# Optimization experiments

Hardware: AMD Instinct MI355X
Metric: run time of the kernel (lower is better)

Reference implementation:

```python
import jax, jax.numpy as jnp
import numpy as np

N, DIM = 65536, 512

def setup_inputs() -> dict:
    key = jax.random.key(0)
    k1, k2, k3 = jax.random.split(key, 3)
    x = jax.random.normal(k1, (N, DIM), dtype=jnp.float32)
    x_fit = jax.random.normal(k2, (N, DIM), dtype=jnp.float32)
    # Module registers S_inv = eye(dim); add a small symmetric PSD perturbation
    # so the matrix is non-trivial while staying well-conditioned.
    A = jax.random.normal(k3, (DIM, DIM), dtype=jnp.float32) / jnp.float32(DIM)
    S_inv = jnp.eye(DIM, dtype=jnp.float32) + A @ A.T
    return {"x": x, "x_fit": x_fit, "S_inv": S_inv}

def reference(x, x_fit, S_inv):
    # Squared Mahalanobis distance per row:
    # diag(delta @ S_inv @ delta.T) == sum((delta @ S_inv) * delta, axis=-1)
    delta = x - x_fit                      # [N, d]
    return jnp.einsum('nd,de,ne->n', delta, S_inv, delta)  # [N]
```

## Files before the change

kernel.cpp:

```cpp
#include <hip/hip_runtime.h>
#include <stdint.h>

#define DIM 512
#define ROWS_PER_BLOCK 64
#define N_CHUNKS 32
#define CHUNK_BYTES 8192
#define WS_BYTES (N_CHUNKS * CHUNK_BYTES)

typedef __attribute__((ext_vector_type(4))) float f32x4;
typedef __attribute__((ext_vector_type(2))) float f32x2;
typedef __attribute__((ext_vector_type(4))) int   i32x4;

static __device__ __forceinline__ int kperm(int kk, int q) {
  int g = q >> 3, j = q & 7;
  int r = (j < 4) ? (g * 4 + j) : (16 + g * 4 + (j - 4));
  return kk * 32 + r;
}

__global__ void prep_R(const float* __restrict__ S, uint32_t* __restrict__ ws) {
  int idx = blockIdx.x * blockDim.x + threadIdx.x;
  if (idx >= WS_BYTES / 4) return;
  int b     = idx * 4;
  int chunk = b >> 13;
  int e_l   = (b >> 9) & 15;
  int inrow = b & 511;
  int slot  = inrow >> 4;
  int bia   = inrow & 15;
  int la    = (slot - e_l) & 31;
  int P = la >> 2, g = la & 3;
  int e = chunk * 16 + e_l;
  float v[4];
#pragma unroll
  for (int t = 0; t < 4; ++t) {
    int bb = bia + t;
    int j  = bb & 7;
    int kk = 2 * P + (bb >> 3);
    int k  = kperm(kk, g * 8 + j);
    v[t] = 64.0f * (S[k * DIM + e] - (k == e ? 1.0f : 0.0f));
  }
  int w = __builtin_amdgcn_cvt_pk_fp8_f32(v[0], v[1], 0, false);
  w     = __builtin_amdgcn_cvt_pk_fp8_f32(v[2], v[3], w, true);
  ws[idx] = (uint32_t)w;
}

static __device__ __forceinline__ void stage_chunk(const uint32_t* __restrict__ ws,
                                                   int eb, char* dst, int tid) {
  const uint32_t* src = ws + (size_t)eb * (CHUNK_BYTES / 4);
#pragma unroll
  for (int r = 0; r < 2; ++r) {
    int idx = r * 256 + tid;
    __builtin_amdgcn_global_load_lds(
        (const __attribute__((address_space(1))) void*)(src + idx * 4),
        (__attribute__((address_space(3))) void*)(dst + idx * 16),
        16, 0, 0);
  }
}

template <int KK>
struct P0 {
  static __device__ __forceinline__ void run(const float* __restrict__ xr,
                                             const float* __restrict__ fr,
                                             int g, long long (&fragL)[16], float& sumsq) {
    const float4 a0 = *(const float4*)(xr + KK * 32 + 4 * g);
    const float4 b0 = *(const float4*)(fr + KK * 32 + 4 * g);
    const float4 a1 = *(const float4*)(xr + KK * 32 + 16 + 4 * g);
    const float4 b1 = *(const float4*)(fr + KK * 32 + 16 + 4 * g);
    float d0 = a0.x - b0.x, d1 = a0.y - b0.y, d2 = a0.z - b0.z, d3 = a0.w - b0.w;
    float d4 = a1.x - b1.x, d5 = a1.y - b1.y, d6 = a1.z - b1.z, d7 = a1.w - b1.w;
    sumsq += d0*d0 + d1*d1 + d2*d2 + d3*d3 + d4*d4 + d5*d5 + d6*d6 + d7*d7;
    int lo = __builtin_amdgcn_cvt_pk_fp8_f32(d0, d1, 0, false);
    lo     = __builtin_amdgcn_cvt_pk_fp8_f32(d2, d3, lo, true);
    int hi = __builtin_amdgcn_cvt_pk_fp8_f32(d4, d5, 0, false);
    hi     = __builtin_amdgcn_cvt_pk_fp8_f32(d6, d7, hi, true);
    fragL[KK] = (long long)(((unsigned long long)(unsigned)hi << 32) | (unsigned)lo);
    P0<KK + 1>::run(xr, fr, g, fragL, sumsq);
  }
};
template <>
struct P0<16> {
  static __device__ __forceinline__ void run(const float*, const float*, int,
                                             long long (&)[16], float&) {}
};

template <int P>
struct KLoop {
  static __device__ __forceinline__ void run(const char* __restrict__ rowbase,
                                             int g, int m,
                                             const long long (&fragL)[16],
                                             f32x4& c0, f32x4& c1) {
    int off = ((4 * P + g + m) & 31) * 16;
    i32x4 a = *(const i32x4*)(rowbase + off);
    long long A0 = (long long)(((unsigned long long)(unsigned)a[1] << 32) | (unsigned)a[0]);
    long long A1 = (long long)(((unsigned long long)(unsigned)a[3] << 32) | (unsigned)a[2]);
    c0 = __builtin_amdgcn_mfma_f32_16x16x32_fp8_fp8(A0, fragL[2 * P],     c0, 0, 0, 0);
    c1 = __builtin_amdgcn_mfma_f32_16x16x32_fp8_fp8(A1, fragL[2 * P + 1], c1, 0, 0, 0);
    KLoop<P + 1>::run(rowbase, g, m, fragL, c0, c1);
  }
};
template <>
struct KLoop<8> {
  static __device__ __forceinline__ void run(const char*, int, int,
                                             const long long (&)[16], f32x4&, f32x4&) {}
};

template <int EB>
struct ChunkLoop {
  static __device__ __forceinline__ void run(const uint32_t* __restrict__ ws,
                                             char* sA0, char* sA1,
                                             int tid, int m, int g,
                                             const long long (&fragL)[16], float& part) {
    char* cur = (EB & 1) ? sA1 : sA0;
    char* nxt = (EB & 1) ? sA0 : sA1;
    if (EB + 1 < N_CHUNKS) stage_chunk(ws, EB + 1, nxt, tid);

    f32x4 c0 = {0.f, 0.f, 0.f, 0.f}, c1 = {0.f, 0.f, 0.f, 0.f};
    KLoop<0>::run(cur + m * 512, g, m, fragL, c0, c1);

    constexpr int kk = EB >> 1;
    int src = (int)(fragL[kk] >> ((EB & 1) * 32));
    f32x2 f01 = __builtin_amdgcn_cvt_pk_f32_fp8(src, false);
    f32x2 f23 = __builtin_amdgcn_cvt_pk_f32_fp8(src, true);
    part += (c0[0] + c1[0]) * f01[0] + (c0[1] + c1[1]) * f01[1]
          + (c0[2] + c1[2]) * f23[0] + (c0[3] + c1[3]) * f23[1];

    __syncthreads();
    ChunkLoop<EB + 1>::run(ws, sA0, sA1, tid, m, g, fragL, part);
  }
};
template <>
struct ChunkLoop<N_CHUNKS> {
  static __device__ __forceinline__ void run(const uint32_t*, char*, char*, int, int, int,
                                             const long long (&)[16], float&) {}
};

__global__ __launch_bounds__(256, 2)
void mahal_main(const float* __restrict__ X, const float* __restrict__ XF,
                const uint32_t* __restrict__ ws, float* __restrict__ out) {
  __shared__ __align__(16) char sA[2][CHUNK_BYTES];

  const int tid  = threadIdx.x;
  const int lane = tid & 63;
  const int wv   = tid >> 6;
  const int m    = lane & 15;
  const int g    = lane >> 4;
  const int row  = blockIdx.x * ROWS_PER_BLOCK + wv * 16 + m;

  const float* xr = X  + (size_t)row * DIM;
  const float* fr = XF + (size_t)row * DIM;

  stage_chunk(ws, 0, sA[0], tid);

  long long fragL[16];
  float sumsq = 0.f;
  P0<0>::run(xr, fr, g, fragL, sumsq);
  sumsq += __shfl_xor(sumsq, 16);
  sumsq += __shfl_xor(sumsq, 32);

  __syncthreads();

  float part = 0.f;
  ChunkLoop<0>::run(ws, sA[0], sA[1], tid, m, g, fragL, part);

  part += __shfl_xor(part, 16);
  part += __shfl_xor(part, 32);
  if (g == 0) out[row] = sumsq + part * 0.015625f;
}

__global__ void mahal_naive(const float* __restrict__ X, const float* __restrict__ XF,
                            const float* __restrict__ S, float* __restrict__ out, int n) {
  int row = blockIdx.x * blockDim.x + threadIdx.x;
  if (row >= n) return;
  const float* xr = X + (size_t)row * DIM;
  const float* fr = XF + (size_t)row * DIM;
  float acc = 0.f;
  for (int d = 0; d < DIM; ++d) {
    float dd = xr[d] - fr[d];
    float inner = 0.f;
    for (int e = 0; e < DIM; ++e) inner += S[d * DIM + e] * (xr[e] - fr[e]);
    acc += dd * inner;
  }
  out[row] = acc;
}

extern "C" void kernel_launch(void* const* d_in, const int* in_sizes, int n_in,
                              void* d_out, int out_size, void* d_ws, size_t ws_size,
                              hipStream_t stream) {
  const float* X  = (const float*)d_in[0];
  const float* XF = (const float*)d_in[1];
  const float* S  = (const float*)d_in[2];
  float* out = (float*)d_out;
  const int N = in_sizes[0] / DIM;

  if (ws_size < (size_t)WS_BYTES || (N % ROWS_PER_BLOCK) != 0) {
    mahal_naive<<<(N + 63) / 64, 64, 0, stream>>>(X, XF, S, out, N);
    return;
  }

  uint32_t* ws = (uint32_t*)d_ws;
  prep_R<<<(WS_BYTES / 4 + 255) / 256, 256, 0, stream>>>(S, ws);
  mahal_main<<<N / ROWS_PER_BLOCK, 256, 0, stream>>>(X, XF, ws, out);
}
```

Baseline: 306.7 us.

## Load fp8 matrix chunks directly into registers per wave instead of LDS staging

```diff
diff --git a/kernel.cpp b/kernel.cpp
--- a/kernel.cpp
+++ b/kernel.cpp
@@ -2,7 +2,7 @@
 #include <stdint.h>
 
 #define DIM 512
-#define ROWS_PER_BLOCK 64
+#define ROWS_PER_BLOCK 16
 #define N_CHUNKS 32
 #define CHUNK_BYTES 8192
 #define WS_BYTES (N_CHUNKS * CHUNK_BYTES)
@@ -43,19 +43,6 @@
   ws[idx] = (uint32_t)w;
 }
 
-static __device__ __forceinline__ void stage_chunk(const uint32_t* __restrict__ ws,
-                                                   int eb, char* dst, int tid) {
-  const uint32_t* src = ws + (size_t)eb * (CHUNK_BYTES / 4);
-#pragma unroll
-  for (int r = 0; r < 2; ++r) {
-    int idx = r * 256 + tid;
-    __builtin_amdgcn_global_load_lds(
-        (const __attribute__((address_space(1))) void*)(src + idx * 4),
-        (__attribute__((address_space(3))) void*)(dst + idx * 16),
-        16, 0, 0);
-  }
-}
-
 template <int KK>
 struct P0 {
   static __device__ __forceinline__ void run(const float* __restrict__ xr,
@@ -83,38 +70,49 @@
 };
 
 template <int P>
-struct KLoop {
-  static __device__ __forceinline__ void run(const char* __restrict__ rowbase,
-                                             int g, int m,
-                                             const long long (&fragL)[16],
-                                             f32x4& c0, f32x4& c1) {
-    int off = ((4 * P + g + m) & 31) * 16;
-    i32x4 a = *(const i32x4*)(rowbase + off);
-    long long A0 = (long long)(((unsigned long long)(unsigned)a[1] << 32) | (unsigned)a[0]);
-    long long A1 = (long long)(((unsigned long long)(unsigned)a[3] << 32) | (unsigned)a[2]);
-    c0 = __builtin_amdgcn_mfma_f32_16x16x32_fp8_fp8(A0, fragL[2 * P],     c0, 0, 0, 0);
-    c1 = __builtin_amdgcn_mfma_f32_16x16x32_fp8_fp8(A1, fragL[2 * P + 1], c1, 0, 0, 0);
-    KLoop<P + 1>::run(rowbase, g, m, fragL, c0, c1);
+struct ALoad {
+  static __device__ __forceinline__ void run(const char* __restrict__ cbase,
+                                             int rot, i32x4 (&A)[8]) {
+    int off = ((4 * P + rot) & 31) * 16;
+    A[P] = *(const i32x4*)(cbase + off);
+    ALoad<P + 1>::run(cbase, rot, A);
   }
 };
 template <>
-struct KLoop<8> {
-  static __device__ __forceinline__ void run(const char*, int, int,
+struct ALoad<8> {
+  static __device__ __forceinline__ void run(const char*, int, i32x4 (&)[8]) {}
+};
+
+template <int P>
+struct AMfma {
+  static __device__ __forceinline__ void run(const i32x4 (&A)[8],
+                                             const long long (&fragL)[16],
+                                             f32x4& c0, f32x4& c1) {
+    long long A0 = (long long)(((unsigned long long)(unsigned)A[P][1] << 32) | (unsigned)A[P][0]);
+    long long A1 = (long long)(((unsigned long long)(unsigned)A[P][3] << 32) | (unsigned)A[P][2]);
+    c0 = __builtin_amdgcn_mfma_f32_16x16x32_fp8_fp8(A0, fragL[2 * P],     c0, 0, 0, 0);
+    c1 = __builtin_amdgcn_mfma_f32_16x16x32_fp8_fp8(A1, fragL[2 * P + 1], c1, 0, 0, 0);
+    AMfma<P + 1>::run(A, fragL, c0, c1);
+  }
+};
+template <>
+struct AMfma<8> {
+  static __device__ __forceinline__ void run(const i32x4 (&)[8],
                                              const long long (&)[16], f32x4&, f32x4&) {}
 };
 
 template <int EB>
 struct ChunkLoop {
-  static __device__ __forceinline__ void run(const uint32_t* __restrict__ ws,
-                                             char* sA0, char* sA1,
-                                             int tid, int m, int g,
-                                             const long long (&fragL)[16], float& part) {
-    char* cur = (EB & 1) ? sA1 : sA0;
-    char* nxt = (EB & 1) ? sA0 : sA1;
-    if (EB + 1 < N_CHUNKS) stage_chunk(ws, EB + 1, nxt, tid);
+  static __device__ __forceinline__ void run(const char* __restrict__ wsb,
+                                             int rot,
+                                             const long long (&fragL)[16],
+                                             i32x4 (&cur)[8], i32x4 (&nxt)[8],
+                                             float& part) {
+    if constexpr (EB + 1 < N_CHUNKS)
+      ALoad<0>::run(wsb + (size_t)(EB + 1) * CHUNK_BYTES, rot, nxt);
 
     f32x4 c0 = {0.f, 0.f, 0.f, 0.f}, c1 = {0.f, 0.f, 0.f, 0.f};
-    KLoop<0>::run(cur + m * 512, g, m, fragL, c0, c1);
+    AMfma<0>::run(cur, fragL, c0, c1);
 
     constexpr int kk = EB >> 1;
     int src = (int)(fragL[kk] >> ((EB & 1) * 32));
@@ -123,32 +121,26 @@
     part += (c0[0] + c1[0]) * f01[0] + (c0[1] + c1[1]) * f01[1]
           + (c0[2] + c1[2]) * f23[0] + (c0[3] + c1[3]) * f23[1];
 
-    __syncthreads();
-    ChunkLoop<EB + 1>::run(ws, sA0, sA1, tid, m, g, fragL, part);
+    ChunkLoop<EB + 1>::run(wsb, rot, fragL, nxt, cur, part);
   }
 };
 template <>
 struct ChunkLoop<N_CHUNKS> {
-  static __device__ __forceinline__ void run(const uint32_t*, char*, char*, int, int, int,
-                                             const long long (&)[16], float&) {}
+  static __device__ __forceinline__ void run(const char*, int,
+                                             const long long (&)[16],
+                                             i32x4 (&)[8], i32x4 (&)[8], float&) {}
 };
 
-__global__ __launch_bounds__(256, 2)
+__global__ __launch_bounds__(64, 3)
 void mahal_main(const float* __restrict__ X, const float* __restrict__ XF,
                 const uint32_t* __restrict__ ws, float* __restrict__ out) {
-  __shared__ __align__(16) char sA[2][CHUNK_BYTES];
-
-  const int tid  = threadIdx.x;
-  const int lane = tid & 63;
-  const int wv   = tid >> 6;
+  const int lane = threadIdx.x;
   const int m    = lane & 15;
   const int g    = lane >> 4;
-  const int row  = blockIdx.x * ROWS_PER_BLOCK + wv * 16 + m;
+  const int row  = blockIdx.x * ROWS_PER_BLOCK + m;
 
   const float* xr = X  + (size_t)row * DIM;
   const float* fr = XF + (size_t)row * DIM;
-
-  stage_chunk(ws, 0, sA[0], tid);
 
   long long fragL[16];
   float sumsq = 0.f;
@@ -156,10 +148,14 @@
   sumsq += __shfl_xor(sumsq, 16);
   sumsq += __shfl_xor(sumsq, 32);
 
-  __syncthreads();
+  const char* wsb = (const char*)ws + m * 512;
+  const int rot = g + m;
+
+  i32x4 A[8], B[8];
+  ALoad<0>::run(wsb, rot, A);
 
   float part = 0.f;
-  ChunkLoop<0>::run(ws, sA[0], sA[1], tid, m, g, fragL, part);
+  ChunkLoop<0>::run(wsb, rot, fragL, A, B, part);
 
   part += __shfl_xor(part, 16);
   part += __shfl_xor(part, 32);
@@ -198,5 +194,5 @@
 
   uint32_t* ws = (uint32_t*)d_ws;
   prep_R<<<(WS_BYTES / 4 + 255) / 256, 256, 0, stream>>>(S, ws);
-  mahal_main<<<N / ROWS_PER_BLOCK, 256, 0, stream>>>(X, XF, ws, out);
+  mahal_main<<<N / ROWS_PER_BLOCK, 64, 0, stream>>>(X, XF, ws, out);
 }
```

After: 389.2 us. +26.9%, slower.

## Deepen LDS staging of S chunks to four buffers with three-ahead prefetch

Applied to the files above, without the earlier changes.

```diff
diff --git a/kernel.cpp b/kernel.cpp
--- a/kernel.cpp
+++ b/kernel.cpp
@@ -6,6 +6,8 @@
 #define N_CHUNKS 32
 #define CHUNK_BYTES 8192
 #define WS_BYTES (N_CHUNKS * CHUNK_BYTES)
+#define N_BUF 4
+#define PREFETCH 3
 
 typedef __attribute__((ext_vector_type(4))) float f32x4;
 typedef __attribute__((ext_vector_type(2))) float f32x2;
@@ -106,15 +108,24 @@
 template <int EB>
 struct ChunkLoop {
   static __device__ __forceinline__ void run(const uint32_t* __restrict__ ws,
-                                             char* sA0, char* sA1,
+                                             char* __restrict__ sbase,
                                              int tid, int m, int g,
                                              const long long (&fragL)[16], float& part) {
-    char* cur = (EB & 1) ? sA1 : sA0;
-    char* nxt = (EB & 1) ? sA0 : sA1;
-    if (EB + 1 < N_CHUNKS) stage_chunk(ws, EB + 1, nxt, tid);
-
+    if constexpr (EB <= N_CHUNKS - 3)
+      asm volatile("s_waitcnt vmcnt(4) lgkmcnt(0)" ::: "memory");
+    else if constexpr (EB == N_CHUNKS - 2)
+      asm volatile("s_waitcnt vmcnt(2) lgkmcnt(0)" ::: "memory");
+    else
+      asm volatile("s_waitcnt vmcnt(0) lgkmcnt(0)" ::: "memory");
+    __builtin_amdgcn_s_barrier();
+
+    if constexpr (EB + PREFETCH < N_CHUNKS)
+      stage_chunk(ws, EB + PREFETCH,
+                  sbase + ((EB + PREFETCH) & (N_BUF - 1)) * CHUNK_BYTES, tid);
+
+    const char* rowbase = sbase + (EB & (N_BUF - 1)) * CHUNK_BYTES + m * 512;
     f32x4 c0 = {0.f, 0.f, 0.f, 0.f}, c1 = {0.f, 0.f, 0.f, 0.f};
-    KLoop<0>::run(cur + m * 512, g, m, fragL, c0, c1);
+    KLoop<0>::run(rowbase, g, m, fragL, c0, c1);
 
     constexpr int kk = EB >> 1;
     int src = (int)(fragL[kk] >> ((EB & 1) * 32));
@@ -123,20 +134,19 @@
     part += (c0[0] + c1[0]) * f01[0] + (c0[1] + c1[1]) * f01[1]
           + (c0[2] + c1[2]) * f23[0] + (c0[3] + c1[3]) * f23[1];
 
-    __syncthreads();
-    ChunkLoop<EB + 1>::run(ws, sA0, sA1, tid, m, g, fragL, part);
+    ChunkLoop<EB + 1>::run(ws, sbase, tid, m, g, fragL, part);
   }
 };
 template <>
 struct ChunkLoop<N_CHUNKS> {
-  static __device__ __forceinline__ void run(const uint32_t*, char*, char*, int, int, int,
+  static __device__ __forceinline__ void run(const uint32_t*, char*, int, int, int,
                                              const long long (&)[16], float&) {}
 };
 
 __global__ __launch_bounds__(256, 2)
 void mahal_main(const float* __restrict__ X, const float* __restrict__ XF,
                 const uint32_t* __restrict__ ws, float* __restrict__ out) {
-  __shared__ __align__(16) char sA[2][CHUNK_BYTES];
+  __shared__ __align__(16) char sA[N_BUF][CHUNK_BYTES];
 
   const int tid  = threadIdx.x;
   const int lane = tid & 63;
@@ -149,6 +159,8 @@
   const float* fr = XF + (size_t)row * DIM;
 
   stage_chunk(ws, 0, sA[0], tid);
+  stage_chunk(ws, 1, sA[1], tid);
+  stage_chunk(ws, 2, sA[2], tid);
 
   long long fragL[16];
   float sumsq = 0.f;
@@ -156,10 +168,8 @@
   sumsq += __shfl_xor(sumsq, 16);
   sumsq += __shfl_xor(sumsq, 32);
 
-  __syncthreads();
-
   float part = 0.f;
-  ChunkLoop<0>::run(ws, sA[0], sA[1], tid, m, g, fragL, part);
+  ChunkLoop<0>::run(ws, &sA[0][0], tid, m, g, fragL, part);
 
   part += __shfl_xor(part, 16);
   part += __shfl_xor(part, 32);
```

Measured after the change: 304.7 us. No clear change (-0.7%).
